# Optimization experiments

Measured on AMD Instinct MI355X. Metric: run time of the kernel, lower is better.

The kernel has to match this reference:

```python
import jax, jax.numpy as jnp
import numpy as np

HIDDEN = 1024
N_HEAD = 16
HEAD_DIM = HIDDEN // N_HEAD  # 64
BATCH = 1
SEQ = 4096
THETA = 10000.0


def _rope_cos_sin(seq_len, head_dim, dtype=jnp.float32):
    # freqs[t, j] = t / theta^(2j/dim), j in [0, dim/2)
    inv_freq = 1.0 / (THETA ** (jnp.arange(0, head_dim, 2, dtype=dtype) / head_dim))
    t = jnp.arange(seq_len, dtype=dtype)
    freqs = jnp.outer(t, inv_freq)           # [S, D/2]
    return jnp.cos(freqs), jnp.sin(freqs)


def _apply_rope(x, cos, sin):
    # x: [B, S, H, D]; pairs (x[...,2j], x[...,2j+1]) rotated by angle freqs[t, j]
    x2 = x.reshape(*x.shape[:-1], -1, 2)       # [B, S, H, D/2, 2]
    x_re, x_im = x2[..., 0], x2[..., 1]
    c = cos[None, :, None, :]                   # [1, S, 1, D/2]
    s = sin[None, :, None, :]
    out_re = x_re * c - x_im * s
    out_im = x_re * s + x_im * c
    out = jnp.stack([out_re, out_im], axis=-1)  # [B, S, H, D/2, 2]
    return out.reshape(x.shape)


def setup_inputs() -> dict:
    key = jax.random.key(0)
    kx, kq, kk, kv = jax.random.split(key, 4)
    scale = 1.0 / np.sqrt(HIDDEN)
    return {
        "x": jax.random.normal(kx, (BATCH, SEQ, HIDDEN), dtype=jnp.float32),
        "wq": jax.random.normal(kq, (HIDDEN, HIDDEN), dtype=jnp.float32) * scale,
        "wk": jax.random.normal(kk, (HIDDEN, HIDDEN), dtype=jnp.float32) * scale,
        "wv": jax.random.normal(kv, (HIDDEN, HIDDEN), dtype=jnp.float32) * scale,
    }


def reference(x, wq, wk, wv):
    B, S, _ = x.shape
    # torch nn.Linear(no bias): y = x @ W.T
    xq = (x @ wq.T).reshape(B, S, N_HEAD, HEAD_DIM).astype(jnp.float32)
    xk = (x @ wk.T).reshape(B, S, N_HEAD, HEAD_DIM).astype(jnp.float32)
    xv = (x @ wv.T).reshape(B, S, N_HEAD, HEAD_DIM).astype(jnp.float32)

    cos, sin = _rope_cos_sin(S, HEAD_DIM)
    q = _apply_rope(xq, cos, sin)
    k = _apply_rope(xk, cos, sin)

    # [B, H, S, S] scores, no causal mask (matches source)
    scores = jnp.einsum("bqhd,bkhd->bhqk", q, k) / jnp.sqrt(
        jnp.asarray(HEAD_DIM, dtype=q.dtype))
    attn = jax.nn.softmax(scores, axis=-1)
    out = jnp.einsum("bhqk,bkhd->bqhd", attn, xv)  # [B, S, H, D]
    return out.reshape(B, S, N_HEAD * HEAD_DIM)
```

## Files before the change

### kernel.cpp

```cpp
#include <hip/hip_runtime.h>
#include <stdint.h>


#define SEQLEN 4096
#define NHEAD 16
#define HDIM 64

typedef __bf16 bf16x8 __attribute__((ext_vector_type(8)));
typedef float f32x4 __attribute__((ext_vector_type(4)));
typedef float f32x16 __attribute__((ext_vector_type(16)));

__device__ __forceinline__ unsigned short f2bf(float f) {
  union { float f; unsigned int u; } v; v.f = f;
  unsigned int r = v.u + 0x7FFFu + ((v.u >> 16) & 1u);
  return (unsigned short)(r >> 16);
}
__device__ __forceinline__ unsigned int pkc(float lo, float hi) {
  union { __bf16 b[2]; unsigned int u; } z;
  z.b[0] = (__bf16)lo; z.b[1] = (__bf16)hi;
  return z.u;
}
__device__ __forceinline__ bf16x8 as_bf(uint4 v) { return __builtin_bit_cast(bf16x8, v); }
__device__ __forceinline__ f32x4 mfma16(bf16x8 a, bf16x8 b, f32x4 c) {
  return __builtin_amdgcn_mfma_f32_16x16x32_bf16(a, b, c, 0, 0, 0);
}
__device__ __forceinline__ f32x16 mfma32(bf16x8 a, bf16x8 b, f32x16 c) {
  return __builtin_amdgcn_mfma_f32_32x32x16_bf16(a, b, c, 0, 0, 0);
}
__device__ __forceinline__ uint2 mku2(unsigned x, unsigned y) {
  uint2 r; r.x = x; r.y = y; return r;
}
__device__ __forceinline__ void gll16(const void* g, void* l) {
  __builtin_amdgcn_global_load_lds(
      (const __attribute__((address_space(1))) void*)g,
      (__attribute__((address_space(3))) void*)l, 16, 0, 0);
}

__global__ __launch_bounds__(256) void k_prep(
    const float* __restrict__ x, const float* __restrict__ wq,
    const float* __restrict__ wk, const float* __restrict__ wv,
    unsigned short* __restrict__ xbf, unsigned short* __restrict__ wbf,
    float2* __restrict__ ctst) {
  const int NX = SEQLEN * 1024 / 4;
  const int NW = 1024 * 1024 / 4;
  if (blockIdx.x < 7168) {
    int i = blockIdx.x * 256 + threadIdx.x;
    float4 v;
    unsigned short* dst;
    int di;
    if (i < NX) {
      v = ((const float4*)x)[i]; dst = xbf; di = i;
    } else {
      int j = i - NX;
      const float4* src = (const float4*)((j < NW) ? wq : (j < 2 * NW) ? wk : wv);
      v = src[j & (NW - 1)];
      dst = wbf; di = j;
    }
    ushort4 o; o.x = f2bf(v.x); o.y = f2bf(v.y); o.z = f2bf(v.z); o.w = f2bf(v.w);
    ((ushort4*)dst)[di] = o;
  } else {
    int i = (blockIdx.x - 7168) * 256 + threadIdx.x;
    int s = i >> 5, j = i & 31;
    double inv = exp(-(double)j * 0.28782313662425572);
    double a = (double)s * inv;
    float2 cs; cs.x = (float)cos(a); cs.y = (float)sin(a);
    ctst[i] = cs;
  }
}

__global__ __launch_bounds__(256) void k_gemm(
    const unsigned short* __restrict__ xbf, const unsigned short* __restrict__ wbf,
    const float2* __restrict__ ctst,
    unsigned short* __restrict__ qbf, unsigned short* __restrict__ kbf,
    unsigned short* __restrict__ vT) {
  __shared__ __align__(16) unsigned short As[2][128 * 32];
  __shared__ __align__(16) unsigned short Bs[2][128 * 32];
  const int t = threadIdx.x;
  const int bn = blockIdx.x, bm = blockIdx.y;
  const int lane = t & 63, wave = t >> 6;
  const int r = lane & 15, g = lane >> 4;
  const int wm = wave >> 1, wn = wave & 1;

  const int c0 = 2 * wave, c1 = 2 * wave + 1;
  const int srowA = lane >> 2, sb = (lane & 3) * 16;
  const char* gA0 = (const char*)xbf + (size_t)(bm * 128 + 16 * c0 + srowA) * 2048 + sb;
  const char* gA1 = (const char*)xbf + (size_t)(bm * 128 + 16 * c1 + srowA) * 2048 + sb;
  const char* gB0 = (const char*)wbf + (size_t)(bn * 128 + 16 * c0 + srowA) * 2048 + sb;
  const char* gB1 = (const char*)wbf + (size_t)(bn * 128 + 16 * c1 + srowA) * 2048 + sb;

  gll16(gA0, (char*)As[0] + c0 * 1024);
  gll16(gA1, (char*)As[0] + c1 * 1024);
  gll16(gB0, (char*)Bs[0] + c0 * 1024);
  gll16(gB1, (char*)Bs[0] + c1 * 1024);
  gA0 += 64; gA1 += 64; gB0 += 64; gB1 += 64;

  f32x4 zero4 = {0.f, 0.f, 0.f, 0.f};
  f32x4 acc[4][4];
#pragma unroll
  for (int m = 0; m < 4; ++m)
#pragma unroll
    for (int n = 0; n < 4; ++n) acc[m][n] = zero4;

  for (int kk = 0; kk < 32; ++kk) {
    __syncthreads();
    if (kk < 31) {
      char* Ad = (char*)As[(kk + 1) & 1];
      char* Bd = (char*)Bs[(kk + 1) & 1];
      gll16(gA0, Ad + c0 * 1024);
      gll16(gA1, Ad + c1 * 1024);
      gll16(gB0, Bd + c0 * 1024);
      gll16(gB1, Bd + c1 * 1024);
      gA0 += 64; gA1 += 64; gB0 += 64; gB1 += 64;
    }
    const char* Ac = (const char*)As[kk & 1];
    const char* Bc = (const char*)Bs[kk & 1];
    bf16x8 af[4], bfr[4];
#pragma unroll
    for (int m = 0; m < 4; ++m)
      af[m] = as_bf(*(const uint4*)(Ac + (wm * 64 + m * 16 + r) * 64 + g * 16));
#pragma unroll
    for (int n = 0; n < 4; ++n)
      bfr[n] = as_bf(*(const uint4*)(Bc + (wn * 64 + n * 16 + r) * 64 + g * 16));
#pragma unroll
    for (int m = 0; m < 4; ++m)
#pragma unroll
      for (int n = 0; n < 4; ++n)
        acc[m][n] = mfma16(af[m], bfr[n], acc[m][n]);
  }

  const int matid = bn >> 3;
#pragma unroll
  for (int m = 0; m < 4; ++m) {
    const int row0 = bm * 128 + wm * 64 + m * 16 + 4 * g;
#pragma unroll
    for (int n = 0; n < 4; ++n) {
      const int col = bn * 128 + wn * 64 + n * 16 + r;
      const int d = col & 63;
      const int hh = (col >> 6) & 15;
      if (matid < 2) {
        const int jdx = (col >> 1) & 31;
        const float sgn = (col & 1) ? 1.0f : -1.0f;
        unsigned short* dst = (matid == 0) ? qbf : kbf;
        const float qs = (matid == 0) ? 0.18033688011112042f : 1.0f;
#pragma unroll
        for (int j = 0; j < 4; ++j) {
          float v = acc[m][n][j];
          float p = __shfl_xor(v, 1);
          int srow = row0 + j;
          float2 cs = ctst[srow * 32 + jdx];
          float o = (v * cs.x + p * cs.y * sgn) * qs;
          dst[(size_t)srow * 1024 + (hh * 64 + d)] = f2bf(o);
        }
      } else {
        ushort4 o;
        o.x = f2bf(acc[m][n][0]); o.y = f2bf(acc[m][n][1]);
        o.z = f2bf(acc[m][n][2]); o.w = f2bf(acc[m][n][3]);
        *(ushort4*)&vT[((size_t)(hh * 64 + d)) * SEQLEN + row0] = o;
      }
    }
  }
}

__global__ __launch_bounds__(512) void k_attn(
    const unsigned short* __restrict__ qbf, const unsigned short* __restrict__ kbf,
    const unsigned short* __restrict__ vT, float* __restrict__ out) {
  __shared__ __align__(16) char smem[33280];
  const int t = threadIdx.x;
  const int b = blockIdx.x;
  const int work = (b & 7) * 64 + (b >> 3);
  const int h = work >> 5;
  const int qb = work & 31;
  const int lane = t & 63, wave = t >> 6;
  const int qw = wave & 3, hf = wave >> 2;
  const int li = lane & 31, hi = lane >> 5;
  const int q0 = qb * 128 + qw * 32;
  const int HB = hf * 16384;

  bf16x8 qf[4];
#pragma unroll
  for (int c = 0; c < 4; ++c)
    qf[c] = as_bf(*(const uint4*)((const char*)qbf +
              (size_t)(q0 + li) * 2048 + h * 128 + c * 32 + hi * 16));

  f32x16 z16 = {0.f};
  f32x16 acc[2];
  acc[0] = z16; acc[1] = z16;
  float l4[4] = {0.f, 0.f, 0.f, 0.f};

  const int mmK = (li & 15) ^ (hi << 1);
  int kra[4];
#pragma unroll
  for (int c = 0; c < 4; ++c)
    kra[c] = HB + li * 128 + ((((4 * c) ^ mmK)) << 3);
  const int mmV = (li & 15) ^ hi;
  int vra[2][2];
#pragma unroll
  for (int dt = 0; dt < 2; ++dt)
#pragma unroll
    for (int kc = 0; kc < 2; ++kc)
      vra[dt][kc] = HB + 8192 + li * 128 + ((((dt * 8 + 4 * kc) ^ mmV)) << 3);

  const int tt = t & 255;
  const int kr = tt >> 3, c8 = tt & 7;
  const int vd = tt >> 2, c4 = tt & 3;
  const int wka = HB + kr * 128 + ((((2 * c8) ^ (kr & 15))) << 3);
  const int wva = HB + 8192 + (vd & 31) * 128 +
                  (((((vd >> 5) * 8 + 2 * c4) ^ (vd & 15))) << 3);

  const char* pK = (const char*)kbf + h * 128 +
                   (size_t)(hf * 2048 + kr) * 2048 + c8 * 16;
  const char* pV = (const char*)vT + (size_t)h * HDIM * SEQLEN * 2 +
                   (size_t)vd * 8192 + hf * 4096 + c4 * 16;

  uint4 rk, rv;
#define LD_KV32                                       \
  rk = *(const uint4*)pK; rv = *(const uint4*)pV;     \
  pK += 32 * 2048; pV += 64;

  LD_KV32

#pragma unroll 2
  for (int j = 0; j < 64; ++j) {
    const int JB = (j & 1) * 4096;
    *(uint2*)(smem + (wka + JB)) = mku2(rk.x, rk.y);
    *(uint2*)(smem + ((wka ^ 8) + JB)) = mku2(rk.z, rk.w);
    *(uint2*)(smem + (wva + JB)) = mku2(rv.x, rv.y);
    *(uint2*)(smem + ((wva ^ 8) + JB)) = mku2(rv.z, rv.w);
    __syncthreads();
    if (j < 63) { LD_KV32 }

    f32x16 sT = z16;
    __builtin_amdgcn_s_setprio(1);
#pragma unroll
    for (int c = 0; c < 4; ++c) {
      uint2 a0 = *(const uint2*)(smem + (kra[c] + JB));
      uint2 a1 = *(const uint2*)(smem + ((kra[c] ^ 8) + JB));
      uint4 ku; ku.x = a0.x; ku.y = a0.y; ku.z = a1.x; ku.w = a1.y;
      sT = mfma32(as_bf(ku), qf[c], sT);
    }
    __builtin_amdgcn_s_setprio(0);

    bf16x8 vf[2][2];
#pragma unroll
    for (int dt = 0; dt < 2; ++dt)
#pragma unroll
      for (int kc = 0; kc < 2; ++kc) {
        uint2 lo = *(const uint2*)(smem + (vra[dt][kc] + JB));
        uint2 hi2 = *(const uint2*)(smem + ((vra[dt][kc] ^ 16) + JB));
        uint4 vv; vv.x = lo.x; vv.y = lo.y; vv.z = hi2.x; vv.w = hi2.y;
        vf[dt][kc] = as_bf(vv);
      }

#pragma unroll
    for (int i = 0; i < 16; ++i) sT[i] = __builtin_amdgcn_exp2f(sT[i]);

#pragma unroll
    for (int i = 0; i < 4; ++i)
      l4[i] += (sT[i] + sT[i + 4]) + (sT[i + 8] + sT[i + 12]);

    bf16x8 pfr[2];
#pragma unroll
    for (int kc = 0; kc < 2; ++kc) {
      const int bix = kc * 8;
      uint4 bw;
      bw.x = pkc(sT[bix + 0], sT[bix + 1]);
      bw.y = pkc(sT[bix + 2], sT[bix + 3]);
      bw.z = pkc(sT[bix + 4], sT[bix + 5]);
      bw.w = pkc(sT[bix + 6], sT[bix + 7]);
      pfr[kc] = as_bf(bw);
    }
    __builtin_amdgcn_s_setprio(1);
#pragma unroll
    for (int kc = 0; kc < 2; ++kc) {
      acc[0] = mfma32(vf[0][kc], pfr[kc], acc[0]);
      acc[1] = mfma32(vf[1][kc], pfr[kc], acc[1]);
    }
    __builtin_amdgcn_s_setprio(0);
  }

  float lrun = (l4[0] + l4[1]) + (l4[2] + l4[3]);
  float lhalf = lrun + __shfl_xor(lrun, 32);

  __syncthreads();
  float* shm = (float*)smem;
  if (hf == 1) {
    float* ab = shm + qw * 2048;
#pragma unroll
    for (int dt = 0; dt < 2; ++dt)
#pragma unroll
      for (int i = 0; i < 16; ++i) {
        int d = (i & 3) + 8 * (i >> 2) + 4 * hi + 32 * dt;
        ab[d * 32 + li] = acc[dt][i];
      }
    if (hi == 0) shm[8192 + qw * 32 + li] = lhalf;
  }
  __syncthreads();
  if (hf == 0) {
    float* ab = shm + qw * 2048;
    float l1 = shm[8192 + qw * 32 + li];
    float linv = 1.0f / (lhalf + l1);
#pragma unroll
    for (int dt = 0; dt < 2; ++dt)
#pragma unroll
      for (int i = 0; i < 16; ++i) {
        int d = (i & 3) + 8 * (i >> 2) + 4 * hi + 32 * dt;
        acc[dt][i] = (acc[dt][i] + ab[d * 32 + li]) * linv;
      }
    __asm__ volatile("" ::: "memory");

    float* eb = shm + qw * 2048;
#pragma unroll
    for (int dt = 0; dt < 2; ++dt) {
#pragma unroll
      for (int i = 0; i < 16; ++i)
        eb[li * 33 + ((i & 3) + 8 * (i >> 2) + 4 * hi)] = acc[dt][i];
      __asm__ volatile("" ::: "memory");
#pragma unroll
      for (int it = 0; it < 16; ++it) {
        int q = it * 2 + hi;
        float v = eb[q * 33 + li];
        out[(size_t)(q0 + q) * 1024 + h * 64 + dt * 32 + li] = v;
      }
      __asm__ volatile("" ::: "memory");
    }
  }
}

extern "C" void kernel_launch(void* const* d_in, const int* in_sizes, int n_in,
                              void* d_out, int out_size, void* d_ws, size_t ws_size,
                              hipStream_t stream) {
  const float* x  = (const float*)d_in[0];
  const float* wq = (const float*)d_in[1];
  const float* wk = (const float*)d_in[2];
  const float* wv = (const float*)d_in[3];
  float* out = (float*)d_out;
  char* ws = (char*)d_ws;

  unsigned short* qbf = (unsigned short*)(ws);
  unsigned short* kbf = (unsigned short*)(ws + ((size_t)8 << 20));
  unsigned short* vT  = (unsigned short*)(ws + ((size_t)16 << 20));
  unsigned short* xbf = (unsigned short*)(ws + ((size_t)24 << 20));
  unsigned short* wbf = (unsigned short*)(ws + ((size_t)32 << 20));
  float2* ctst = (float2*)(ws + ((size_t)38 << 20));

  k_prep<<<dim3(7680), dim3(256), 0, stream>>>(x, wq, wk, wv, xbf, wbf, ctst);
  k_gemm<<<dim3(24, 32), dim3(256), 0, stream>>>(xbf, wbf, ctst, qbf, kbf, vT);
  k_attn<<<dim3(512), dim3(512), 0, stream>>>(qbf, kbf, vT, out);
}
```

Measured before the change: 149.1 us.

## Pre-swizzle K/V in GEMM epilogue and stream tiles via direct global-to-LDS loads

```diff
diff --git a/kernel.cpp b/kernel.cpp
--- a/kernel.cpp
+++ b/kernel.cpp
@@ -26,9 +26,6 @@
 }
 __device__ __forceinline__ f32x16 mfma32(bf16x8 a, bf16x8 b, f32x16 c) {
   return __builtin_amdgcn_mfma_f32_32x32x16_bf16(a, b, c, 0, 0, 0);
-}
-__device__ __forceinline__ uint2 mku2(unsigned x, unsigned y) {
-  uint2 r; r.x = x; r.y = y; return r;
 }
 __device__ __forceinline__ void gll16(const void* g, void* l) {
   __builtin_amdgcn_global_load_lds(
@@ -71,8 +68,8 @@
 __global__ __launch_bounds__(256) void k_gemm(
     const unsigned short* __restrict__ xbf, const unsigned short* __restrict__ wbf,
     const float2* __restrict__ ctst,
-    unsigned short* __restrict__ qbf, unsigned short* __restrict__ kbf,
-    unsigned short* __restrict__ vT) {
+    unsigned short* __restrict__ qbf, unsigned short* __restrict__ Kswz,
+    unsigned short* __restrict__ Vswz) {
   __shared__ __align__(16) unsigned short As[2][128 * 32];
   __shared__ __align__(16) unsigned short Bs[2][128 * 32];
   const int t = threadIdx.x;
@@ -140,30 +137,38 @@
       if (matid < 2) {
         const int jdx = (col >> 1) & 31;
         const float sgn = (col & 1) ? 1.0f : -1.0f;
-        unsigned short* dst = (matid == 0) ? qbf : kbf;
         const float qs = (matid == 0) ? 0.18033688011112042f : 1.0f;
 #pragma unroll
         for (int j = 0; j < 4; ++j) {
           float v = acc[m][n][j];
           float p = __shfl_xor(v, 1);
-          int srow = row0 + j;
-          float2 cs = ctst[srow * 32 + jdx];
+          int key = row0 + j;
+          float2 cs = ctst[key * 32 + jdx];
           float o = (v * cs.x + p * cs.y * sgn) * qs;
-          dst[(size_t)srow * 1024 + (hh * 64 + d)] = f2bf(o);
+          if (matid == 0) {
+            qbf[(size_t)key * 1024 + (hh * 64 + d)] = f2bf(o);
+          } else {
+            size_t off = (size_t)hh * 524288 + (size_t)key * 128 +
+                         (size_t)((2 * d) ^ ((key & 15) << 3));
+            *(unsigned short*)((char*)Kswz + off) = f2bf(o);
+          }
         }
       } else {
         ushort4 o;
         o.x = f2bf(acc[m][n][0]); o.y = f2bf(acc[m][n][1]);
         o.z = f2bf(acc[m][n][2]); o.w = f2bf(acc[m][n][3]);
-        *(ushort4*)&vT[((size_t)(hh * 64 + d)) * SEQLEN + row0] = o;
+        size_t off = (size_t)hh * 524288 + (size_t)(row0 >> 5) * 4096 +
+                     (size_t)(d & 31) * 128 +
+                     (size_t)((((d >> 5) * 8 + ((row0 >> 2) & 7)) ^ (d & 15)) << 3);
+        *(ushort4*)((char*)Vswz + off) = o;
       }
     }
   }
 }
 
 __global__ __launch_bounds__(512) void k_attn(
-    const unsigned short* __restrict__ qbf, const unsigned short* __restrict__ kbf,
-    const unsigned short* __restrict__ vT, float* __restrict__ out) {
+    const unsigned short* __restrict__ qbf, const unsigned short* __restrict__ Kswz,
+    const unsigned short* __restrict__ Vswz, float* __restrict__ out) {
   __shared__ __align__(16) char smem[33280];
   const int t = threadIdx.x;
   const int b = blockIdx.x;
@@ -200,34 +205,26 @@
     for (int kc = 0; kc < 2; ++kc)
       vra[dt][kc] = HB + 8192 + li * 128 + ((((dt * 8 + 4 * kc) ^ mmV)) << 3);
 
-  const int tt = t & 255;
-  const int kr = tt >> 3, c8 = tt & 7;
-  const int vd = tt >> 2, c4 = tt & 3;
-  const int wka = HB + kr * 128 + ((((2 * c8) ^ (kr & 15))) << 3);
-  const int wva = HB + 8192 + (vd & 31) * 128 +
-                  (((((vd >> 5) * 8 + 2 * c4) ^ (vd & 15))) << 3);
-
-  const char* pK = (const char*)kbf + h * 128 +
-                   (size_t)(hf * 2048 + kr) * 2048 + c8 * 16;
-  const char* pV = (const char*)vT + (size_t)h * HDIM * SEQLEN * 2 +
-                   (size_t)vd * 8192 + hf * 4096 + c4 * 16;
-
-  uint4 rk, rv;
-#define LD_KV32                                       \
-  rk = *(const uint4*)pK; rv = *(const uint4*)pV;     \
-  pK += 32 * 2048; pV += 64;
-
-  LD_KV32
-
-#pragma unroll 2
+  const char* pK = (const char*)Kswz + (size_t)h * 524288 + (size_t)hf * 262144 +
+                   (size_t)qw * 1024 + (size_t)lane * 16;
+  const char* pV = (const char*)Vswz + (size_t)h * 524288 + (size_t)hf * 262144 +
+                   (size_t)qw * 1024 + (size_t)lane * 16;
+  char* dK = smem + HB + qw * 1024;
+  char* dV = smem + HB + 8192 + qw * 1024;
+
+  gll16(pK, dK);
+  gll16(pV, dV);
+  pK += 4096; pV += 4096;
+
   for (int j = 0; j < 64; ++j) {
+    __syncthreads();
+    if (j < 63) {
+      const int NB = ((j + 1) & 1) * 4096;
+      gll16(pK, dK + NB);
+      gll16(pV, dV + NB);
+      pK += 4096; pV += 4096;
+    }
     const int JB = (j & 1) * 4096;
-    *(uint2*)(smem + (wka + JB)) = mku2(rk.x, rk.y);
-    *(uint2*)(smem + ((wka ^ 8) + JB)) = mku2(rk.z, rk.w);
-    *(uint2*)(smem + (wva + JB)) = mku2(rv.x, rv.y);
-    *(uint2*)(smem + ((wva ^ 8) + JB)) = mku2(rv.z, rv.w);
-    __syncthreads();
-    if (j < 63) { LD_KV32 }
 
     f32x16 sT = z16;
     __builtin_amdgcn_s_setprio(1);
@@ -336,14 +333,14 @@
   float* out = (float*)d_out;
   char* ws = (char*)d_ws;
 
-  unsigned short* qbf = (unsigned short*)(ws);
-  unsigned short* kbf = (unsigned short*)(ws + ((size_t)8 << 20));
-  unsigned short* vT  = (unsigned short*)(ws + ((size_t)16 << 20));
-  unsigned short* xbf = (unsigned short*)(ws + ((size_t)24 << 20));
-  unsigned short* wbf = (unsigned short*)(ws + ((size_t)32 << 20));
+  unsigned short* qbf  = (unsigned short*)(ws);
+  unsigned short* Kswz = (unsigned short*)(ws + ((size_t)8 << 20));
+  unsigned short* Vswz = (unsigned short*)(ws + ((size_t)16 << 20));
+  unsigned short* xbf  = (unsigned short*)(ws + ((size_t)24 << 20));
+  unsigned short* wbf  = (unsigned short*)(ws + ((size_t)32 << 20));
   float2* ctst = (float2*)(ws + ((size_t)38 << 20));
 
   k_prep<<<dim3(7680), dim3(256), 0, stream>>>(x, wq, wk, wv, xbf, wbf, ctst);
-  k_gemm<<<dim3(24, 32), dim3(256), 0, stream>>>(xbf, wbf, ctst, qbf, kbf, vT);
-  k_attn<<<dim3(512), dim3(512), 0, stream>>>(qbf, kbf, vT, out);
-}
+  k_gemm<<<dim3(24, 32), dim3(256), 0, stream>>>(xbf, wbf, ctst, qbf, Kswz, Vswz);
+  k_attn<<<dim3(512), dim3(512), 0, stream>>>(qbf, Kswz, Vswz, out);
+}
```

Result: slower. 154.7 us (+3.8%).

## Stream K/V tiles to LDS with direct global_load_lds and 16-byte swizzle

Applied to the files above, without the earlier changes.

```diff
diff --git a/kernel.cpp b/kernel.cpp
--- a/kernel.cpp
+++ b/kernel.cpp
@@ -26,9 +26,6 @@
 }
 __device__ __forceinline__ f32x16 mfma32(bf16x8 a, bf16x8 b, f32x16 c) {
   return __builtin_amdgcn_mfma_f32_32x32x16_bf16(a, b, c, 0, 0, 0);
-}
-__device__ __forceinline__ uint2 mku2(unsigned x, unsigned y) {
-  uint2 r; r.x = x; r.y = y; return r;
 }
 __device__ __forceinline__ void gll16(const void* g, void* l) {
   __builtin_amdgcn_global_load_lds(
@@ -187,56 +184,47 @@
   acc[0] = z16; acc[1] = z16;
   float l4[4] = {0.f, 0.f, 0.f, 0.f};
 
-  const int mmK = (li & 15) ^ (hi << 1);
   int kra[4];
 #pragma unroll
   for (int c = 0; c < 4; ++c)
-    kra[c] = HB + li * 128 + ((((4 * c) ^ mmK)) << 3);
-  const int mmV = (li & 15) ^ hi;
+    kra[c] = HB + li * 128 + (((2 * c + hi) ^ (li & 7)) << 4);
   int vra[2][2];
 #pragma unroll
   for (int dt = 0; dt < 2; ++dt)
 #pragma unroll
     for (int kc = 0; kc < 2; ++kc)
-      vra[dt][kc] = HB + 8192 + li * 128 + ((((dt * 8 + 4 * kc) ^ mmV)) << 3);
-
-  const int tt = t & 255;
-  const int kr = tt >> 3, c8 = tt & 7;
-  const int vd = tt >> 2, c4 = tt & 3;
-  const int wka = HB + kr * 128 + ((((2 * c8) ^ (kr & 15))) << 3);
-  const int wva = HB + 8192 + (vd & 31) * 128 +
-                  (((((vd >> 5) * 8 + 2 * c4) ^ (vd & 15))) << 3);
-
+      vra[dt][kc] = HB + 8192 + li * 128 + (((4 * dt + 2 * kc) ^ (li & 7)) << 4) + hi * 8;
+
+  const int srow = qw * 8 + (lane >> 3);
+  const int gg = lane & 7;
+  const int og = gg ^ (srow & 7);
   const char* pK = (const char*)kbf + h * 128 +
-                   (size_t)(hf * 2048 + kr) * 2048 + c8 * 16;
-  const char* pV = (const char*)vT + (size_t)h * HDIM * SEQLEN * 2 +
-                   (size_t)vd * 8192 + hf * 4096 + c4 * 16;
-
-  uint4 rk, rv;
-#define LD_KV32                                       \
-  rk = *(const uint4*)pK; rv = *(const uint4*)pV;     \
+                   (size_t)(hf * 2048 + srow) * 2048 + og * 16;
+  const char* pV = (const char*)vT + (size_t)(h * 64 + (og >> 2) * 32 + srow) * 8192 +
+                   hf * 4096 + (og & 3) * 16;
+  char* dK = smem + HB + qw * 1024;
+  char* dV = smem + HB + 8192 + qw * 1024;
+
+  gll16(pK, dK);
+  gll16(pV, dV);
   pK += 32 * 2048; pV += 64;
 
-  LD_KV32
-
-#pragma unroll 2
   for (int j = 0; j < 64; ++j) {
+    __syncthreads();
+    if (j < 63) {
+      const int NB = ((j + 1) & 1) * 4096;
+      gll16(pK, dK + NB);
+      gll16(pV, dV + NB);
+      pK += 32 * 2048; pV += 64;
+    }
     const int JB = (j & 1) * 4096;
-    *(uint2*)(smem + (wka + JB)) = mku2(rk.x, rk.y);
-    *(uint2*)(smem + ((wka ^ 8) + JB)) = mku2(rk.z, rk.w);
-    *(uint2*)(smem + (wva + JB)) = mku2(rv.x, rv.y);
-    *(uint2*)(smem + ((wva ^ 8) + JB)) = mku2(rv.z, rv.w);
-    __syncthreads();
-    if (j < 63) { LD_KV32 }
 
     f32x16 sT = z16;
     __builtin_amdgcn_s_setprio(1);
 #pragma unroll
     for (int c = 0; c < 4; ++c) {
-      uint2 a0 = *(const uint2*)(smem + (kra[c] + JB));
-      uint2 a1 = *(const uint2*)(smem + ((kra[c] ^ 8) + JB));
-      uint4 ku; ku.x = a0.x; ku.y = a0.y; ku.z = a1.x; ku.w = a1.y;
-      sT = mfma32(as_bf(ku), qf[c], sT);
+      bf16x8 kf = as_bf(*(const uint4*)(smem + (kra[c] + JB)));
+      sT = mfma32(kf, qf[c], sT);
     }
     __builtin_amdgcn_s_setprio(0);
 
```

Result: faster. 144.9 us, median of 2 (-2.8%).
